# Optimization experiments

Hardware: AMD Instinct MI355X
Metric: run time of the kernel (lower is better)

Reference implementation:

```python
import jax, jax.numpy as jnp
import numpy as np

B, N, FIN, HID, HEADS, LAYERS = 2048, 62, 128, 512, 8, 3
FOUT = HID // HEADS  # 64


def setup_inputs() -> dict:
    key = jax.random.key(0)
    ks = jax.random.split(key, 12)
    x = jax.random.normal(ks[0], (B, N, FIN), dtype=jnp.float32)
    adj = jax.random.randint(ks[1], (B, N, N), 0, 2, dtype=jnp.int32)
    # BatchNorm1d(62) params (eval mode, running stats)
    bn_gamma = jax.random.normal(ks[2], (N,), dtype=jnp.float32) * 0.1 + 1.0
    bn_beta = jax.random.normal(ks[3], (N,), dtype=jnp.float32) * 0.1
    bn_mean = jax.random.normal(ks[4], (N,), dtype=jnp.float32) * 0.1
    bn_var = jax.random.uniform(ks[5], (N,), dtype=jnp.float32, minval=0.5, maxval=1.5)
    # input MLP
    W_mlp = jax.random.normal(ks[6], (FIN, HID), dtype=jnp.float32) / np.sqrt(FIN)
    b_mlp = jnp.zeros((HID,), dtype=jnp.float32)
    # GAT params: one W [HID, FOUT] and one a [2*FOUT] per (layer, head)
    W_gat = jax.random.normal(ks[7], (LAYERS, HEADS, HID, FOUT), dtype=jnp.float32) / np.sqrt(HID)
    a_gat = jax.random.normal(ks[8], (LAYERS, HEADS, 2 * FOUT), dtype=jnp.float32) / np.sqrt(2 * FOUT)
    # output head
    W_out = jax.random.normal(ks[9], (HID, 3), dtype=jnp.float32) / np.sqrt(HID)
    b_out = jnp.zeros((3,), dtype=jnp.float32)
    return {
        "x": x, "adj": adj,
        "bn_gamma": bn_gamma, "bn_beta": bn_beta, "bn_mean": bn_mean, "bn_var": bn_var,
        "W_mlp": W_mlp, "b_mlp": b_mlp,
        "W_gat": W_gat, "a_gat": a_gat,
        "W_out": W_out, "b_out": b_out,
    }


def reference(x, adj, bn_gamma, bn_beta, bn_mean, bn_var, W_mlp, b_mlp, W_gat, a_gat, W_out, b_out):
    eps = 1e-5
    alpha = 0.2  # LeakyReLU slope
    # BatchNorm1d over the node dim (C=62), eval mode
    xb = (x - bn_mean[None, :, None]) * (bn_gamma / jnp.sqrt(bn_var + eps))[None, :, None] + bn_beta[None, :, None]
    h_x = xb @ W_mlp + b_mlp  # [B, N, HID]
    mask = adj > 0  # [B, N, N]
    n_layers, n_heads, _, f_out = W_gat.shape
    for l in range(n_layers):
        # all heads at once: h [H, B, N, FOUT]
        h = jnp.einsum('bnf,hfd->hbnd', h_x, W_gat[l])
        a1 = a_gat[l][:, :f_out]   # multiplies the repeat(1,N,1) part -> h_j
        a2 = a_gat[l][:, f_out:]   # multiplies the repeat(1,1,N) part -> h_i
        f1 = jnp.einsum('hbnd,hd->hbn', h, a1)  # per-node source term
        f2 = jnp.einsum('hbnd,hd->hbn', h, a2)  # per-node dest term
        # e[h,b,i,j] = leaky(a2.h_i + a1.h_j)  (matches cat/repeat layout)
        e = jax.nn.leaky_relu(f2[:, :, :, None] + f1[:, :, None, :], alpha)
        e = jnp.where(mask[None], e, jnp.float32(-9e15))
        # torch F.softmax(attention, dim=1) on [B,N,N] -> axis=2 here (the i axis)
        att = jax.nn.softmax(e, axis=2)
        hp = jnp.einsum('hbij,hbjd->hbid', att, h)
        hp = jax.nn.elu(hp)
        # concat heads on feature dim -> [B, N, HID]
        h_x = jnp.transpose(hp, (1, 2, 0, 3)).reshape(h_x.shape[0], h_x.shape[1], n_heads * f_out)
    pooled = jnp.sum(h_x, axis=1)  # [B, HID]
    logits = pooled @ W_out + b_out  # [B, 3]
    return jax.nn.log_softmax(logits, axis=-1)
```

## Files before the change

### kernel.cpp

```cpp
#include <hip/hip_runtime.h>
#include <cstdint>
#include <cstddef>

#define B_ 2048
#define N_ 62
#define FIN_ 128
#define HID_ 512
#define HEADS_ 8
#define FOUT_ 64
#define LAYERS_ 3
#define M_ (B_*N_)

typedef __bf16 bf16x8 __attribute__((ext_vector_type(8)));
typedef __bf16 bf16x4 __attribute__((ext_vector_type(4)));
typedef float  f32x4  __attribute__((ext_vector_type(4)));
typedef unsigned short u16;

#define LOG2E 1.4426950408889634f

#if __has_builtin(__builtin_amdgcn_exp2f)
#define EXP2F(x) __builtin_amdgcn_exp2f(x)
#else
#define EXP2F(x) exp2f(x)
#endif
#if __has_builtin(__builtin_amdgcn_logf)
#define LOG2F(x) __builtin_amdgcn_logf(x)
#else
#define LOG2F(x) log2f(x)
#endif

static __device__ __forceinline__ u16 f2bf(float f) {
    union { float f; uint32_t u; } v; v.f = f;
    uint32_t u = v.u;
    return (u16)((u + 0x7fffu + ((u >> 16) & 1u)) >> 16);
}
static __device__ __forceinline__ float bf2f(u16 s) {
    union { uint32_t u; float f; } v; v.u = ((uint32_t)s) << 16;
    return v.f;
}
static __device__ __forceinline__ float rdlane(float v, int l) {
    union { float f; int i; } a, b; a.f = v;
    b.i = __builtin_amdgcn_readlane(a.i, l);
    return b.f;
}
static __device__ __forceinline__ bf16x4 pack4(f32x4 v) {
    bf16x4 o;
    o[0] = (__bf16)v[0]; o[1] = (__bf16)v[1];
    o[2] = (__bf16)v[2]; o[3] = (__bf16)v[3];
    return o;
}

__global__ __launch_bounds__(256) void repack_w(
    const float* __restrict__ Wm, const float* __restrict__ Wg,
    u16* __restrict__ wmlp_t, u16* __restrict__ wgat2)
{
    int idx = blockIdx.x * 256 + threadIdx.x;
    const int T1 = HID_ * FIN_;
    const int T2 = LAYERS_ * HEADS_ * 64 * HID_;
    if (idx < T1) {
        int n = idx / FIN_, k = idx % FIN_;
        wmlp_t[idx] = f2bf(Wm[k * HID_ + n]);
    } else if (idx < T1 + T2) {
        int j = idx - T1;
        int lh = j / (64 * HID_);
        int r  = j % (64 * HID_);
        int n = r / HID_, k = r % HID_;
        wgat2[j] = f2bf(Wg[((size_t)lh * HID_ + k) * FOUT_ + n]);
    }
}

__global__ __launch_bounds__(256) void build_masks(
    const int* __restrict__ adj, uint64_t* __restrict__ masks,
    uint64_t* __restrict__ masksT)
{
    __shared__ uint32_t m32[128];
    const int b = blockIdx.x, tid = threadIdx.x;
    if (tid < 128) m32[tid] = 0;
    __syncthreads();
    const int* a = adj + (size_t)b * N_ * N_;
    for (int idx = tid; idx < N_ * N_; idx += 256) {
        int i = idx / N_, j = idx % N_;
        if (a[idx] > 0) atomicOr(&m32[i * 2 + (j >> 5)], 1u << (j & 31));
    }
    __syncthreads();
    if (tid < 128) ((uint32_t*)(masks + (size_t)b * 64))[tid] = m32[tid];
    if (tid < 64) {
        int j = tid;
        uint64_t c = 0;
        for (int i = 0; i < N_; i++) {
            uint64_t bit = (m32[i * 2 + (j >> 5)] >> (j & 31)) & 1u;
            c |= bit << i;
        }
        masksT[(size_t)b * 64 + j] = c;
    }
}

#define S_R  72
#define RSZ  4608
#define S_X  136
#define X0   27648

__global__ __launch_bounds__(512, 4) void gat_fused(
    const float* __restrict__ x,
    const float* __restrict__ bng, const float* __restrict__ bnb,
    const float* __restrict__ bnm, const float* __restrict__ bnv,
    const u16* __restrict__ wmlp_t, const float* __restrict__ bm,
    const u16* __restrict__ wgat2, const float* __restrict__ ag,
    const uint64_t* __restrict__ masks, const uint64_t* __restrict__ masksT,
    const float* __restrict__ Wout, const float* __restrict__ bout,
    float* __restrict__ out)
{
    __shared__ __align__(16) u16 buf[36864];
    __shared__ uint64_t msk[64];
    __shared__ __align__(16) float fstat[1544];
    float* F1 = fstat;
    float* F2 = fstat + 512;
    float* LS = fstat + 1024;

    const int tid = threadIdx.x, b = blockIdx.x;
    const int wave = tid >> 6, lane = tid & 63;
    const int lr = lane & 15, lq = lane >> 4;
    const int w64 = wave * 64;
    const int wreg = wave * RSZ;

    const uint64_t cm = masksT[(size_t)b * 64 + lane];
    const uint32_t cml = (uint32_t)cm, cmh = (uint32_t)(cm >> 32);

    {
        const float* xg = x + (size_t)b * N_ * FIN_;
        for (int idx = tid; idx < 2048; idx += 512) {
            int n = idx >> 5, kq = idx & 31;
            bf16x4 o = {(__bf16)0.f, (__bf16)0.f, (__bf16)0.f, (__bf16)0.f};
            if (n < N_) {
                float s = bng[n] * rsqrtf(bnv[n] + 1e-5f);
                float sh = bnb[n] - bnm[n] * s;
                float4 v = *(const float4*)(xg + n * FIN_ + kq * 4);
                o[0] = (__bf16)(v.x * s + sh); o[1] = (__bf16)(v.y * s + sh);
                o[2] = (__bf16)(v.z * s + sh); o[3] = (__bf16)(v.w * s + sh);
            }
            *(bf16x4*)&buf[X0 + n * S_X + kq * 4] = o;
        }
        if (tid < 64) msk[tid] = (tid < N_) ? masks[(size_t)b * 64 + tid] : 0ull;
    }
    __syncthreads();

    {
        f32x4 acc[4][4];
#pragma unroll
        for (int mt = 0; mt < 4; mt++)
#pragma unroll
            for (int nt = 0; nt < 4; nt++) acc[mt][nt] = (f32x4){0.f, 0.f, 0.f, 0.f};
        const int c0 = w64;
#pragma unroll 1
        for (int kt = 0; kt < 4; kt++) {
            int k0 = kt * 32;
            bf16x8 xf[4];
#pragma unroll
            for (int nt = 0; nt < 4; nt++)
                xf[nt] = *(const bf16x8*)&buf[X0 + (nt * 16 + lr) * S_X + k0 + lq * 8];
#pragma unroll
            for (int mt = 0; mt < 4; mt++) {
                bf16x8 wf = *(const bf16x8*)(wmlp_t + (size_t)(c0 + mt * 16 + lr) * FIN_ + k0 + lq * 8);
#pragma unroll
                for (int nt = 0; nt < 4; nt++)
                    acc[mt][nt] = __builtin_amdgcn_mfma_f32_16x16x32_bf16(
                        wf, xf[nt], acc[mt][nt], 0, 0, 0);
            }
        }
        __syncthreads();
        f32x4 bl[4];
#pragma unroll
        for (int mt = 0; mt < 4; mt++)
            bl[mt] = *(const f32x4*)&bm[c0 + mt * 16 + lq * 4];
#pragma unroll
        for (int mt = 0; mt < 4; mt++)
#pragma unroll
            for (int nt = 0; nt < 4; nt++) {
                int node = nt * 16 + lr;
                if (node < N_)
                    *(bf16x4*)&buf[wreg + node * S_R + mt * 16 + lq * 4] =
                        pack4(acc[mt][nt] + bl[mt]);
            }
        if (lane < 16) {
            uint4 z = {0u, 0u, 0u, 0u};
            *(uint4*)&buf[wreg + (N_ + (lane >> 3)) * S_R + (lane & 7) * 8] = z;
        }
    }
    __syncthreads();

#pragma unroll 1
    for (int l = 0; l < LAYERS_; l++) {
        const u16* wp = wgat2 + (size_t)(l * HEADS_ + wave) * 64 * HID_;

        f32x4 acc[4][4];
#pragma unroll
        for (int mt = 0; mt < 4; mt++)
#pragma unroll
            for (int nt = 0; nt < 4; nt++) acc[mt][nt] = (f32x4){0.f, 0.f, 0.f, 0.f};
#pragma unroll 1
        for (int kt = 0; kt < 16; kt++) {
            int koff = (kt >> 1) * RSZ + (kt & 1) * 32 + lq * 8;
            bf16x8 af[4];
#pragma unroll
            for (int mt = 0; mt < 4; mt++)
                af[mt] = *(const bf16x8*)&buf[koff + (mt * 16 + lr) * S_R];
#pragma unroll
            for (int nt = 0; nt < 4; nt++) {
                bf16x8 bfr = *(const bf16x8*)(wp + (size_t)(nt * 16 + lr) * HID_ + kt * 32 + lq * 8);
#pragma unroll
                for (int mt = 0; mt < 4; mt++)
                    acc[mt][nt] = __builtin_amdgcn_mfma_f32_16x16x32_bf16(
                        af[mt], bfr, acc[mt][nt], 0, 0, 0);
            }
        }

        {
            float a1v[4], a2v[4];
            const float* agl = ag + (size_t)(l * HEADS_ + wave) * 128;
#pragma unroll
            for (int nt = 0; nt < 4; nt++) {
                a1v[nt] = agl[nt * 16 + lr] * LOG2E;
                a2v[nt] = agl[64 + nt * 16 + lr] * LOG2E;
            }
            float p1v[16], p2v[16];
#pragma unroll
            for (int mt = 0; mt < 4; mt++)
#pragma unroll
                for (int r = 0; r < 4; r++) {
                    float s1 = 0.f, s2 = 0.f;
#pragma unroll
                    for (int nt = 0; nt < 4; nt++) {
                        float hv = acc[mt][nt][r];
                        s1 = fmaf(hv, a1v[nt], s1);
                        s2 = fmaf(hv, a2v[nt], s2);
                    }
                    p1v[mt * 4 + r] = s1;
                    p2v[mt * 4 + r] = s2;
                }
#pragma unroll
            for (int c = 0; c < 8; c++) {
                float tA = __shfl_xor(p1v[c], 8, 64);
                float tB = __shfl_xor(p1v[c + 8], 8, 64);
                p1v[c] = (lr & 8) ? (p1v[c + 8] + tB) : (p1v[c] + tA);
                float uA = __shfl_xor(p2v[c], 8, 64);
                float uB = __shfl_xor(p2v[c + 8], 8, 64);
                p2v[c] = (lr & 8) ? (p2v[c + 8] + uB) : (p2v[c] + uA);
            }
#pragma unroll
            for (int c = 0; c < 4; c++) {
                float tA = __shfl_xor(p1v[c], 4, 64);
                float tB = __shfl_xor(p1v[c + 4], 4, 64);
                p1v[c] = (lr & 4) ? (p1v[c + 4] + tB) : (p1v[c] + tA);
                float uA = __shfl_xor(p2v[c], 4, 64);
                float uB = __shfl_xor(p2v[c + 4], 4, 64);
                p2v[c] = (lr & 4) ? (p2v[c + 4] + uB) : (p2v[c] + uA);
            }
#pragma unroll
            for (int c = 0; c < 2; c++) {
                float tA = __shfl_xor(p1v[c], 2, 64);
                float tB = __shfl_xor(p1v[c + 2], 2, 64);
                p1v[c] = (lr & 2) ? (p1v[c + 2] + tB) : (p1v[c] + tA);
                float uA = __shfl_xor(p2v[c], 2, 64);
                float uB = __shfl_xor(p2v[c + 2], 2, 64);
                p2v[c] = (lr & 2) ? (p2v[c + 2] + uB) : (p2v[c] + uA);
            }
            {
                float tA = __shfl_xor(p1v[0], 1, 64);
                float tB = __shfl_xor(p1v[1], 1, 64);
                float f1fin = (lr & 1) ? (p1v[1] + tB) : (p1v[0] + tA);
                float uA = __shfl_xor(p2v[0], 1, 64);
                float uB = __shfl_xor(p2v[1], 1, 64);
                float f2fin = (lr & 1) ? (p2v[1] + uB) : (p2v[0] + uA);
                int node = (lr >> 2) * 16 + lq * 4 + (lr & 3);
                F1[w64 + node] = f1fin;
                F2[w64 + node] = f2fin;
            }
        }

        __syncthreads();

#pragma unroll
        for (int mt = 0; mt < 4; mt++)
#pragma unroll
            for (int nt = 0; nt < 4; nt++)
                *(bf16x4*)&buf[wreg + (nt * 16 + lr) * S_R + mt * 16 + lq * 4] =
                    pack4(acc[mt][nt]);

        {
            float p1 = F1[w64 + lane];
            float p2 = F2[w64 + lane];
            float pm = (lane < N_) ? p2 : -3.0e38f;
#pragma unroll
            for (int off = 32; off; off >>= 1) pm = fmaxf(pm, __shfl_xor(pm, off, 64));
            float vm = pm + p1;
            float m = fmaxf(vm, 0.2f * vm);
            float s0 = 0.f, s1 = 0.f;
#pragma unroll
            for (int i = 0; i < N_; i += 2) {
                float fa = rdlane(p2, i), fb = rdlane(p2, i + 1);
                float va = fa + p1, vb = fb + p1;
                va = fmaxf(va, 0.2f * va); vb = fmaxf(vb, 0.2f * vb);
                float ea = EXP2F(va - m), eb = EXP2F(vb - m);
                uint32_t w = (i < 32) ? cml : cmh;
                s0 += ((w >> (i & 31)) & 1u) ? ea : 0.f;
                s1 += ((w >> ((i + 1) & 31)) & 1u) ? eb : 0.f;
            }
            float ssum = fmaxf(s0 + s1, 1e-35f);
            LS[w64 + lane] = m + LOG2F(ssum);
        }

        f32x4 acc2[4][4];
#pragma unroll
        for (int mt = 0; mt < 4; mt++)
#pragma unroll
            for (int it = 0; it < 4; it++) acc2[mt][it] = (f32x4){0.f, 0.f, 0.f, 0.f};
        float f2v[4];
#pragma unroll
        for (int it = 0; it < 4; it++) f2v[it] = F2[w64 + it * 16 + lr];
#pragma unroll
        for (int kt = 0; kt < 2; kt++) {
            int j0 = kt * 32 + lq * 8;
            bf16x8 pf[4];
#pragma unroll
            for (int h = 0; h < 2; h++) {
                f32x4 f1h = *(const f32x4*)&F1[w64 + j0 + 4 * h];
                f32x4 lsh = *(const f32x4*)&LS[w64 + j0 + 4 * h];
#pragma unroll
                for (int it = 0; it < 4; it++) {
                    uint64_t mi = msk[it * 16 + lr];
                    uint32_t sh = ((uint32_t)(mi >> (kt * 32))) >> (lq * 8 + 4 * h);
#pragma unroll
                    for (int t = 0; t < 4; t++) {
                        float v = f2v[it] + f1h[t];
                        v = fmaxf(v, 0.2f * v);
                        float p = EXP2F(v - lsh[t]);
                        p = ((sh >> t) & 1u) ? p : 0.f;
                        pf[it][4 * h + t] = (__bf16)p;
                    }
                }
            }
#pragma unroll
            for (int mt = 0; mt < 4; mt++) {
                bf16x8 ha = *(const bf16x8*)&buf[wreg + (mt * 16 + lr) * S_R + kt * 32 + lq * 8];
#pragma unroll
                for (int it = 0; it < 4; it++)
                    acc2[mt][it] = __builtin_amdgcn_mfma_f32_16x16x32_bf16(
                        ha, pf[it], acc2[mt][it], 0, 0, 0);
            }
        }

#pragma unroll
        for (int mt = 0; mt < 4; mt++)
#pragma unroll
            for (int it = 0; it < 4; it++) {
                int i = it * 16 + lr;
                f32x4 e;
#pragma unroll
                for (int r = 0; r < 4; r++) {
                    float v = acc2[mt][it][r];
                    e[r] = v > 0.f ? v : EXP2F(v * LOG2E) - 1.f;
                }
                if (i < N_)
                    *(bf16x4*)&buf[wreg + i * S_R + mt * 16 + lq * 4] = pack4(e);
            }
        if (lane < 16) {
            uint4 z = {0u, 0u, 0u, 0u};
            *(uint4*)&buf[wreg + (N_ + (lane >> 3)) * S_R + (lane & 7) * 8] = z;
        }
        __syncthreads();
    }

    {
        float s = 0.f;
#pragma unroll 2
        for (int n = 0; n < N_; n++)
            s += bf2f(buf[(tid >> 6) * RSZ + n * S_R + (tid & 63)]);
        fstat[tid] = s;
    }
    __syncthreads();
    if (tid < 192) {
        int c = tid >> 6, ln = tid & 63;
        float p = 0.f;
#pragma unroll
        for (int k = ln; k < HID_; k += 64) p += fstat[k] * Wout[k * 3 + c];
        for (int off = 32; off > 0; off >>= 1) p += __shfl_down(p, off, 64);
        if (ln == 0) fstat[1536 + c] = p + bout[c];
    }
    __syncthreads();
    if (tid == 0) {
        float l0 = fstat[1536], l1 = fstat[1537], l2 = fstat[1538];
        float mm = fmaxf(l0, fmaxf(l1, l2));
        float s = __expf(l0 - mm) + __expf(l1 - mm) + __expf(l2 - mm);
        float ls = mm + logf(s);
        out[b * 3 + 0] = l0 - ls;
        out[b * 3 + 1] = l1 - ls;
        out[b * 3 + 2] = l2 - ls;
    }
}

extern "C" void kernel_launch(void* const* d_in, const int* in_sizes, int n_in,
                              void* d_out, int out_size, void* d_ws, size_t ws_size,
                              hipStream_t stream)
{
    const float* x   = (const float*)d_in[0];
    const int*   adj = (const int*)d_in[1];
    const float* bng = (const float*)d_in[2];
    const float* bnb = (const float*)d_in[3];
    const float* bnm = (const float*)d_in[4];
    const float* bnv = (const float*)d_in[5];
    const float* Wm  = (const float*)d_in[6];
    const float* bm  = (const float*)d_in[7];
    const float* Wg  = (const float*)d_in[8];
    const float* ag  = (const float*)d_in[9];
    const float* Wo  = (const float*)d_in[10];
    const float* bo  = (const float*)d_in[11];
    float* out = (float*)d_out;

    uint64_t* masks  = (uint64_t*)d_ws;
    uint64_t* masksT = masks + (size_t)B_ * 64;
    u16* wmlp_t = (u16*)(masksT + (size_t)B_ * 64);
    u16* wgat2  = wmlp_t + (size_t)HID_ * FIN_;

    int rep_total = HID_ * FIN_ + LAYERS_ * HEADS_ * 64 * HID_;
    repack_w<<<(rep_total + 255) / 256, 256, 0, stream>>>(Wm, Wg, wmlp_t, wgat2);
    build_masks<<<B_, 256, 0, stream>>>(adj, masks, masksT);

    gat_fused<<<B_, 512, 0, stream>>>(
        x, bng, bnb, bnm, bnv, wmlp_t, bm, wgat2, ag,
        masks, masksT, Wo, bo, out);
}
```

Before: 622.5 us.

## Factor leaky-relu softmax exponentials into products and prefetch weight fragments

```diff
diff --git a/kernel.cpp b/kernel.cpp
--- a/kernel.cpp
+++ b/kernel.cpp
@@ -151,20 +151,33 @@
 #pragma unroll
             for (int nt = 0; nt < 4; nt++) acc[mt][nt] = (f32x4){0.f, 0.f, 0.f, 0.f};
         const int c0 = w64;
+        const u16* wml = wmlp_t + (size_t)(c0 + lr) * FIN_ + lq * 8;
+        bf16x8 wcur[4];
+#pragma unroll
+        for (int mt = 0; mt < 4; mt++)
+            wcur[mt] = *(const bf16x8*)(wml + mt * 16 * FIN_);
 #pragma unroll 1
         for (int kt = 0; kt < 4; kt++) {
+            bf16x8 wnxt[4];
+            if (kt < 3) {
+#pragma unroll
+                for (int mt = 0; mt < 4; mt++)
+                    wnxt[mt] = *(const bf16x8*)(wml + mt * 16 * FIN_ + (kt + 1) * 32);
+            }
             int k0 = kt * 32;
             bf16x8 xf[4];
 #pragma unroll
             for (int nt = 0; nt < 4; nt++)
                 xf[nt] = *(const bf16x8*)&buf[X0 + (nt * 16 + lr) * S_X + k0 + lq * 8];
 #pragma unroll
-            for (int mt = 0; mt < 4; mt++) {
-                bf16x8 wf = *(const bf16x8*)(wmlp_t + (size_t)(c0 + mt * 16 + lr) * FIN_ + k0 + lq * 8);
+            for (int mt = 0; mt < 4; mt++)
 #pragma unroll
                 for (int nt = 0; nt < 4; nt++)
                     acc[mt][nt] = __builtin_amdgcn_mfma_f32_16x16x32_bf16(
-                        wf, xf[nt], acc[mt][nt], 0, 0, 0);
+                        wcur[mt], xf[nt], acc[mt][nt], 0, 0, 0);
+            if (kt < 3) {
+#pragma unroll
+                for (int mt = 0; mt < 4; mt++) wcur[mt] = wnxt[mt];
             }
         }
         __syncthreads();
@@ -177,9 +190,8 @@
 #pragma unroll
             for (int nt = 0; nt < 4; nt++) {
                 int node = nt * 16 + lr;
-                if (node < N_)
-                    *(bf16x4*)&buf[wreg + node * S_R + mt * 16 + lq * 4] =
-                        pack4(acc[mt][nt] + bl[mt]);
+                *(bf16x4*)&buf[wreg + node * S_R + mt * 16 + lq * 4] =
+                    pack4(acc[mt][nt] + bl[mt]);
             }
         if (lane < 16) {
             uint4 z = {0u, 0u, 0u, 0u};
@@ -191,26 +203,39 @@
 #pragma unroll 1
     for (int l = 0; l < LAYERS_; l++) {
         const u16* wp = wgat2 + (size_t)(l * HEADS_ + wave) * 64 * HID_;
+        const u16* wpl = wp + (size_t)lr * HID_ + lq * 8;
 
         f32x4 acc[4][4];
 #pragma unroll
         for (int mt = 0; mt < 4; mt++)
 #pragma unroll
             for (int nt = 0; nt < 4; nt++) acc[mt][nt] = (f32x4){0.f, 0.f, 0.f, 0.f};
+        bf16x8 bcur[4];
+#pragma unroll
+        for (int nt = 0; nt < 4; nt++)
+            bcur[nt] = *(const bf16x8*)(wpl + nt * 16 * HID_);
 #pragma unroll 1
         for (int kt = 0; kt < 16; kt++) {
+            bf16x8 bnxt[4];
+            if (kt < 15) {
+#pragma unroll
+                for (int nt = 0; nt < 4; nt++)
+                    bnxt[nt] = *(const bf16x8*)(wpl + nt * 16 * HID_ + (kt + 1) * 32);
+            }
             int koff = (kt >> 1) * RSZ + (kt & 1) * 32 + lq * 8;
             bf16x8 af[4];
 #pragma unroll
             for (int mt = 0; mt < 4; mt++)
                 af[mt] = *(const bf16x8*)&buf[koff + (mt * 16 + lr) * S_R];
 #pragma unroll
-            for (int nt = 0; nt < 4; nt++) {
-                bf16x8 bfr = *(const bf16x8*)(wp + (size_t)(nt * 16 + lr) * HID_ + kt * 32 + lq * 8);
+            for (int nt = 0; nt < 4; nt++)
 #pragma unroll
                 for (int mt = 0; mt < 4; mt++)
                     acc[mt][nt] = __builtin_amdgcn_mfma_f32_16x16x32_bf16(
-                        af[mt], bfr, acc[mt][nt], 0, 0, 0);
+                        af[mt], bcur[nt], acc[mt][nt], 0, 0, 0);
+            if (kt < 15) {
+#pragma unroll
+                for (int nt = 0; nt < 4; nt++) bcur[nt] = bnxt[nt];
             }
         }
 
@@ -277,6 +302,37 @@
             }
         }
 
+        float pm;
+        {
+            float p1 = F1[w64 + lane];
+            float p2 = F2[w64 + lane];
+            float t = (lane < N_) ? p2 : -3.0e38f;
+#pragma unroll
+            for (int off = 32; off; off >>= 1) t = fmaxf(t, __shfl_xor(t, off, 64));
+            pm = t;
+            float mprime = pm + p1;
+            float m = fmaxf(mprime, 0.2f * mprime);
+            float A  = EXP2F(p2 - pm);
+            float C  = EXP2F(0.2f * (p2 - pm));
+            float be = EXP2F(mprime - m);
+            float de = EXP2F(0.2f * mprime - m);
+            float s0 = 0.f, s1 = 0.f;
+#pragma unroll
+            for (int i = 0; i < N_; i += 2) {
+                float aA = rdlane(A, i), aC = rdlane(C, i);
+                float bA = rdlane(A, i + 1), bC = rdlane(C, i + 1);
+                float ea = fmaxf(aA * be, aC * de);
+                float eb = fmaxf(bA * be, bC * de);
+                uint32_t w = (i < 32) ? cml : cmh;
+                s0 += ((w >> (i & 31)) & 1u) ? ea : 0.f;
+                s1 += ((w >> ((i + 1) & 31)) & 1u) ? eb : 0.f;
+            }
+            float ssum = fmaxf(s0 + s1, 1e-35f);
+            float ls = m + LOG2F(ssum);
+            F1[w64 + lane] = EXP2F(mprime - ls);
+            LS[w64 + lane] = EXP2F(0.2f * mprime - ls);
+        }
+
         __syncthreads();
 
 #pragma unroll
@@ -286,54 +342,33 @@
                 *(bf16x4*)&buf[wreg + (nt * 16 + lr) * S_R + mt * 16 + lq * 4] =
                     pack4(acc[mt][nt]);
 
-        {
-            float p1 = F1[w64 + lane];
-            float p2 = F2[w64 + lane];
-            float pm = (lane < N_) ? p2 : -3.0e38f;
-#pragma unroll
-            for (int off = 32; off; off >>= 1) pm = fmaxf(pm, __shfl_xor(pm, off, 64));
-            float vm = pm + p1;
-            float m = fmaxf(vm, 0.2f * vm);
-            float s0 = 0.f, s1 = 0.f;
-#pragma unroll
-            for (int i = 0; i < N_; i += 2) {
-                float fa = rdlane(p2, i), fb = rdlane(p2, i + 1);
-                float va = fa + p1, vb = fb + p1;
-                va = fmaxf(va, 0.2f * va); vb = fmaxf(vb, 0.2f * vb);
-                float ea = EXP2F(va - m), eb = EXP2F(vb - m);
-                uint32_t w = (i < 32) ? cml : cmh;
-                s0 += ((w >> (i & 31)) & 1u) ? ea : 0.f;
-                s1 += ((w >> ((i + 1) & 31)) & 1u) ? eb : 0.f;
-            }
-            float ssum = fmaxf(s0 + s1, 1e-35f);
-            LS[w64 + lane] = m + LOG2F(ssum);
-        }
-
         f32x4 acc2[4][4];
 #pragma unroll
         for (int mt = 0; mt < 4; mt++)
 #pragma unroll
             for (int it = 0; it < 4; it++) acc2[mt][it] = (f32x4){0.f, 0.f, 0.f, 0.f};
-        float f2v[4];
-#pragma unroll
-        for (int it = 0; it < 4; it++) f2v[it] = F2[w64 + it * 16 + lr];
+        float A4[4], C4[4];
+#pragma unroll
+        for (int it = 0; it < 4; it++) {
+            float f2 = F2[w64 + it * 16 + lr];
+            A4[it] = EXP2F(f2 - pm);
+            C4[it] = EXP2F(0.2f * (f2 - pm));
+        }
 #pragma unroll
         for (int kt = 0; kt < 2; kt++) {
             int j0 = kt * 32 + lq * 8;
             bf16x8 pf[4];
 #pragma unroll
             for (int h = 0; h < 2; h++) {
-                f32x4 f1h = *(const f32x4*)&F1[w64 + j0 + 4 * h];
-                f32x4 lsh = *(const f32x4*)&LS[w64 + j0 + 4 * h];
+                f32x4 bn = *(const f32x4*)&F1[w64 + j0 + 4 * h];
+                f32x4 dn = *(const f32x4*)&LS[w64 + j0 + 4 * h];
 #pragma unroll
                 for (int it = 0; it < 4; it++) {
                     uint64_t mi = msk[it * 16 + lr];
                     uint32_t sh = ((uint32_t)(mi >> (kt * 32))) >> (lq * 8 + 4 * h);
 #pragma unroll
                     for (int t = 0; t < 4; t++) {
-                        float v = f2v[it] + f1h[t];
-                        v = fmaxf(v, 0.2f * v);
-                        float p = EXP2F(v - lsh[t]);
+                        float p = fmaxf(A4[it] * bn[t], C4[it] * dn[t]);
                         p = ((sh >> t) & 1u) ? p : 0.f;
                         pf[it][4 * h + t] = (__bf16)p;
                     }
@@ -360,8 +395,7 @@
                     float v = acc2[mt][it][r];
                     e[r] = v > 0.f ? v : EXP2F(v * LOG2E) - 1.f;
                 }
-                if (i < N_)
-                    *(bf16x4*)&buf[wreg + i * S_R + mt * 16 + lq * 4] = pack4(e);
+                *(bf16x4*)&buf[wreg + i * S_R + mt * 16 + lq * 4] = pack4(e);
             }
         if (lane < 16) {
             uint4 z = {0u, 0u, 0u, 0u};
```

New measurement: 674.0 us. +8.3%, slower.
